# Kernel tuning notes

Hardware: AMD Instinct MI355X
Metric: run time of the kernel (lower is better)

## Reference

```python
import jax, jax.numpy as jnp
import numpy as np

N_HEADS = 16
ALIBI_BIAS_MAX = 8


def _alibi_bias(n_heads, seq_len):
    # MPT build_alibi_bias: bias[h, j] = -(seq_len-1-j) * slope_h, arranged [1,H,1,S]
    pos = jnp.arange(1 - seq_len, 1, dtype=jnp.float32).reshape(1, 1, 1, seq_len)
    m = jnp.arange(1, n_heads + 1, dtype=jnp.float32) * (ALIBI_BIAS_MAX / n_heads)
    slopes = (1.0 / jnp.exp2(m)).reshape(1, n_heads, 1, 1)
    return pos * slopes  # [1,H,1,S]


def setup_inputs() -> dict:
    key = jax.random.key(0)
    k1, k2, k3 = jax.random.split(key, 3)
    B, S, D = 1, 2048, 2048
    x = jax.random.normal(k1, (B, S, D), dtype=jnp.float32)
    # Wqkv: Linear(D, 3D, bias=False); out_proj: Linear(D, D, bias=False)
    w_qkv = jax.random.normal(k2, (3 * D, D), dtype=jnp.float32) * (1.0 / np.sqrt(D))
    w_out = jax.random.normal(k3, (D, D), dtype=jnp.float32) * (1.0 / np.sqrt(D))
    return {"x": x, "w_qkv": w_qkv, "w_out": w_out}


def reference(x, w_qkv, w_out):
    B, S, D = x.shape
    H = N_HEADS
    d = D // H
    qkv = x @ w_qkv.T                              # [B,S,3D]
    q, k, v = jnp.split(qkv, 3, axis=-1)
    q = q.reshape(B, S, H, d).transpose(0, 2, 1, 3)  # [B,H,S,d]
    k = k.reshape(B, S, H, d).transpose(0, 2, 1, 3)
    v = v.reshape(B, S, H, d).transpose(0, 2, 1, 3)
    scale = 1.0 / np.sqrt(d)
    scores = jnp.einsum('bhqd,bhkd->bhqk', q, k) * scale  # [B,H,S,S]
    scores = scores + _alibi_bias(H, S)
    min_val = jnp.finfo(scores.dtype).min
    causal = jnp.tril(jnp.ones((S, S), dtype=bool))
    scores = jnp.where(causal[None, None, :, :], scores, min_val)
    probs = jax.nn.softmax(scores.astype(jnp.float32), axis=-1).astype(q.dtype)
    out = jnp.einsum('bhqk,bhkd->bhqd', probs, v)  # [B,H,S,d]
    out = out.transpose(0, 2, 1, 3).reshape(B, S, D)
    return out @ w_out.T
```

## Files before the change

### kernel.cpp

```cpp
#include <hip/hip_runtime.h>

typedef __bf16 bf16;
typedef __bf16 bf16x8 __attribute__((ext_vector_type(8)));
typedef __bf16 bf16x4 __attribute__((ext_vector_type(4)));
typedef float f32x4 __attribute__((ext_vector_type(4)));

#if __has_builtin(__builtin_amdgcn_exp2f)
#define EXP2(x) __builtin_amdgcn_exp2f(x)
#else
#define EXP2(x) exp2f(x)
#endif

__device__ __forceinline__ void gload_lds16(const void* g, void* l) {
  __builtin_amdgcn_global_load_lds(
      (const __attribute__((address_space(1))) void*)g,
      (__attribute__((address_space(3))) void*)l, 16, 0, 0);
}

__global__ __launch_bounds__(256) void cast_all(const float* __restrict__ x,
                                                const float* __restrict__ wqkv,
                                                const float* __restrict__ wout,
                                                bf16* __restrict__ x_bf,
                                                bf16* __restrict__ wqkv_bf,
                                                bf16* __restrict__ wout_bf) {
  const int b = blockIdx.x;
  const float* src;
  bf16* dst;
  int i;
  if (b < 4096) {
    src = x; dst = x_bf; i = b * 1024 + threadIdx.x * 4;
  } else if (b < 16384) {
    src = wqkv; dst = wqkv_bf; i = (b - 4096) * 1024 + threadIdx.x * 4;
  } else {
    src = wout; dst = wout_bf; i = (b - 16384) * 1024 + threadIdx.x * 4;
  }
  float4 v = *(const float4*)(src + i);
  bf16x4 o = {(bf16)v.x, (bf16)v.y, (bf16)v.z, (bf16)v.w};
  *(bf16x4*)(dst + i) = o;
}

__global__ __launch_bounds__(256) void gemm1_qkv(const bf16* __restrict__ A,
                                                 const bf16* __restrict__ B,
                                                 bf16* __restrict__ qb,
                                                 bf16* __restrict__ kb,
                                                 bf16* __restrict__ vt) {
  constexpr int K = 2048;
  __shared__ bf16 As[128 * 32];
  __shared__ bf16 Bs[128 * 32];
  const int t = threadIdx.x;
  const int w = t >> 6, l = t & 63;
  const int lr = l & 15, lg = l >> 4;
  const int nwg = 768;
  int lin = blockIdx.y * 48 + blockIdx.x;
  lin = (lin & 7) * (nwg >> 3) + (lin >> 3);
  const int bn = lin % 48;
  const int bm = lin / 48;
  const int wr = w >> 1, wc = w & 1;

  f32x4 acc[4][4] = {};
  const int row0 = t >> 2;
  const int cc0 = (t & 3) * 8;

  for (int k0 = 0; k0 < K; k0 += 32) {
#pragma unroll
    for (int r = 0; r < 2; ++r) {
      const int row = r * 64 + row0;
      gload_lds16(A + (size_t)(bm * 128 + row) * K + k0 + cc0,
                  (char*)As + (r * 256 + w * 64) * 16);
      gload_lds16(B + (size_t)(bn * 128 + row) * K + k0 + cc0,
                  (char*)Bs + (r * 256 + w * 64) * 16);
    }
    __syncthreads();
    bf16x8 af[4], bfr[4];
#pragma unroll
    for (int i = 0; i < 4; ++i) {
      af[i] = *(const bf16x8*)((const char*)As + (wr * 64 + i * 16 + lr) * 64 + lg * 16);
      bfr[i] = *(const bf16x8*)((const char*)Bs + (wc * 64 + i * 16 + lr) * 64 + lg * 16);
    }
#pragma unroll
    for (int mi = 0; mi < 4; ++mi)
#pragma unroll
      for (int ni = 0; ni < 4; ++ni)
        acc[mi][ni] = __builtin_amdgcn_mfma_f32_16x16x32_bf16(af[mi], bfr[ni],
                                                              acc[mi][ni], 0, 0, 0);
    __syncthreads();
  }

  const int mb = bm * 128 + wr * 64 + lg * 4;
  const int nb = bn * 128 + wc * 64 + lr;
  if (bn * 128 < 4096) {
    bf16* dst = (bn * 128 < 2048) ? qb : kb;
#pragma unroll
    for (int mi = 0; mi < 4; ++mi) {
      const int mg = mb + mi * 16;
#pragma unroll
      for (int ni = 0; ni < 4; ++ni) {
        const int ng = (nb + ni * 16) & 2047;
#pragma unroll
        for (int rr = 0; rr < 4; ++rr)
          dst[(size_t)(mg + rr) * 2048 + ng] = (bf16)acc[mi][ni][rr];
      }
    }
  } else {
#pragma unroll
    for (int mi = 0; mi < 4; ++mi) {
      const int mg = mb + mi * 16;
#pragma unroll
      for (int ni = 0; ni < 4; ++ni) {
        const int dc = nb + ni * 16 - 4096;
        bf16x4 pk = {(bf16)acc[mi][ni][0], (bf16)acc[mi][ni][1],
                     (bf16)acc[mi][ni][2], (bf16)acc[mi][ni][3]};
        *(bf16x4*)(vt + (size_t)dc * 2048 + mg) = pk;
      }
    }
  }
}

__global__ __launch_bounds__(256) void gemm2_64x128(const bf16* __restrict__ A,
                                                    const bf16* __restrict__ B,
                                                    float* __restrict__ Cf) {
  constexpr int K = 2048, N = 2048;
  __shared__ bf16 As[64 * 32];
  __shared__ bf16 Bs[128 * 32];
  const int t = threadIdx.x;
  const int w = t >> 6, l = t & 63;
  const int lr = l & 15, lg = l >> 4;
  int lin = blockIdx.y * 16 + blockIdx.x;
  lin = (lin & 7) * 64 + (lin >> 3);
  const int bn = lin % 16;
  const int bm = lin / 16;

  f32x4 acc[4][2] = {};

  for (int k0 = 0; k0 < K; k0 += 32) {
    {
      const int row = t >> 2;
      gload_lds16(A + (size_t)(bm * 64 + row) * K + k0 + (t & 3) * 8,
                  (char*)As + (w * 64) * 16);
    }
#pragma unroll
    for (int r = 0; r < 2; ++r) {
      const int c = r * 256 + t;
      const int row = c >> 2;
      gload_lds16(B + (size_t)(bn * 128 + row) * K + k0 + (c & 3) * 8,
                  (char*)Bs + (r * 256 + w * 64) * 16);
    }
    __syncthreads();
    bf16x8 af[4], bfr[2];
#pragma unroll
    for (int i = 0; i < 4; ++i)
      af[i] = *(const bf16x8*)((const char*)As + (i * 16 + lr) * 64 + lg * 16);
#pragma unroll
    for (int i = 0; i < 2; ++i)
      bfr[i] = *(const bf16x8*)((const char*)Bs + (w * 32 + i * 16 + lr) * 64 + lg * 16);
#pragma unroll
    for (int mi = 0; mi < 4; ++mi)
#pragma unroll
      for (int ni = 0; ni < 2; ++ni)
        acc[mi][ni] = __builtin_amdgcn_mfma_f32_16x16x32_bf16(af[mi], bfr[ni],
                                                              acc[mi][ni], 0, 0, 0);
    __syncthreads();
  }

  const int mb = bm * 64 + lg * 4;
  const int nb = bn * 128 + w * 32 + lr;
#pragma unroll
  for (int mi = 0; mi < 4; ++mi) {
    const int mg = mb + mi * 16;
#pragma unroll
    for (int ni = 0; ni < 2; ++ni) {
      const int ng = nb + ni * 16;
#pragma unroll
      for (int rr = 0; rr < 4; ++rr)
        Cf[(size_t)(mg + rr) * N + ng] = acc[mi][ni][rr];
    }
  }
}

__global__ __launch_bounds__(256) void attn_kernel(const bf16* __restrict__ qb,
                                                   const bf16* __restrict__ kb,
                                                   const bf16* __restrict__ vt,
                                                   bf16* __restrict__ out,
                                                   bf16* __restrict__ pA,
                                                   bf16* __restrict__ pB,
                                                   float* __restrict__ ml) {
  constexpr int S = 2048, D = 2048;
  __shared__ bf16 Ks[64 * 128];
  __shared__ bf16 Vs[128 * 64];
  __shared__ bf16 Ps[4][16 * 64];
  const int t = threadIdx.x;
  const int w = t >> 6, l = t & 63;
  const int lr = l & 15, lg = l >> 4;
  const int b = blockIdx.x;

  int h, qt, piece, ns;
  if (b < 1024) {
    const int j = b >> 2;
    h = j & 15; qt = 16 + (j >> 4); piece = b & 3; ns = 4;
  } else if (b < 1280) {
    const int j = (b - 1024) >> 1;
    h = j & 15; qt = 8 + (j >> 4); piece = (b - 1024) & 1; ns = 2;
  } else {
    const int i = b - 1280;
    h = i & 15; qt = i >> 4; piece = 0; ns = 1;
  }
  const bool split = (ns > 1);
  const int q0 = qt * 64;
  const float slope2 = exp2f(-0.5f * (float)(h + 1)) * 1.4426950408889634f;
  const float scale2 = 0.08838834764831845f * 1.4426950408889634f;
  const int W = (int)(24.0f / slope2);
  const int s0 = (q0 > W) ? ((q0 - W) >> 6) : 0;
  const int len = qt + 1 - s0;
  const int start = s0 + (len * piece) / ns;
  const int end = s0 + (len * (piece + 1)) / ns;

  bf16x8 qf[4];
  {
    const bf16* qrow = qb + (size_t)(q0 + w * 16 + lr) * D + h * 128 + lg * 8;
#pragma unroll
    for (int kk = 0; kk < 4; ++kk) qf[kk] = *(const bf16x8*)(qrow + kk * 32);
  }

  f32x4 ob[8] = {};
  float mrow[4] = {-1e30f, -1e30f, -1e30f, -1e30f};
  float lrow[4] = {0.f, 0.f, 0.f, 0.f};

  auto stage = [&](int kv0) {
#pragma unroll
    for (int r = 0; r < 4; ++r) {
      {
        const int krow = r * 16 + (t >> 4);
        const int kcc = t & 15;
        gload_lds16(kb + (size_t)(kv0 + krow) * D + h * 128 + ((kcc ^ (krow & 7)) * 8),
                    (char*)Ks + (r * 256 + w * 64) * 16);
      }
      {
        const int vrow = r * 32 + (t >> 3);
        const int vcc = t & 7;
        gload_lds16(vt + (size_t)(h * 128 + vrow) * S + kv0 + ((vcc ^ (vrow & 7)) * 8),
                    (char*)Vs + (r * 256 + w * 64) * 16);
      }
    }
  };

  for (int tile = start; tile < end; ++tile) {
    const int kv0 = tile << 6;
    stage(kv0);
    __syncthreads();

    f32x4 sc[4] = {};
    __builtin_amdgcn_s_setprio(1);
#pragma unroll
    for (int jb = 0; jb < 4; ++jb) {
      const int row = jb * 16 + lr;
#pragma unroll
      for (int kk = 0; kk < 4; ++kk) {
        const int byte = row * 256 + ((kk * 64 + lg * 16) ^ ((row & 7) << 4));
        bf16x8 kf = *(const bf16x8*)((const char*)Ks + byte);
        sc[jb] = __builtin_amdgcn_mfma_f32_16x16x32_bf16(qf[kk], kf, sc[jb], 0, 0, 0);
      }
    }
    __builtin_amdgcn_s_setprio(0);

    float bias[4];
#pragma unroll
    for (int jb = 0; jb < 4; ++jb)
      bias[jb] = slope2 * (float)(kv0 + jb * 16 + lr - (S - 1));
    const bool diag = (tile == qt);
    float xv[4][4], m2r[4];
#pragma unroll
    for (int rr = 0; rr < 4; ++rr) {
#pragma unroll
      for (int jb = 0; jb < 4; ++jb) {
        float v = fmaf(sc[jb][rr], scale2, bias[jb]);
        if (diag && (jb * 16 + lr > w * 16 + lg * 4 + rr)) v = -1e30f;
        xv[rr][jb] = v;
      }
      float m2 = fmaxf(fmaxf(xv[rr][0], xv[rr][1]), fmaxf(xv[rr][2], xv[rr][3]));
      m2 = fmaxf(m2, __shfl_xor(m2, 1));
      m2 = fmaxf(m2, __shfl_xor(m2, 2));
      m2 = fmaxf(m2, __shfl_xor(m2, 4));
      m2 = fmaxf(m2, __shfl_xor(m2, 8));
      m2r[rr] = m2;
    }
    float need = fmaxf(fmaxf(m2r[0] - mrow[0], m2r[1] - mrow[1]),
                       fmaxf(m2r[2] - mrow[2], m2r[3] - mrow[3]));
    if (!__all(need <= 8.0f)) {
#pragma unroll
      for (int rr = 0; rr < 4; ++rr) {
        const float mnew = fmaxf(mrow[rr], m2r[rr]);
        const float cf = EXP2(mrow[rr] - mnew);
        lrow[rr] *= cf;
        mrow[rr] = mnew;
#pragma unroll
        for (int db = 0; db < 8; ++db) ob[db][rr] *= cf;
      }
    }
    char* pbase = (char*)Ps[w];
#pragma unroll
    for (int rr = 0; rr < 4; ++rr) {
      const int prow = lg * 4 + rr;
      const int sw = (prow & 7) << 4;
      float ps = 0.f;
#pragma unroll
      for (int jb = 0; jb < 4; ++jb) {
        const float p = EXP2(xv[rr][jb] - mrow[rr]);
        *(bf16*)(pbase + ((prow * 128 + jb * 32 + lr * 2) ^ sw)) = (bf16)p;
        ps += p;
      }
      lrow[rr] += ps;
    }

    bf16x8 pf[2];
#pragma unroll
    for (int s = 0; s < 2; ++s)
      pf[s] = *(const bf16x8*)(pbase + ((lr * 128 + s * 64 + lg * 16) ^ ((lr & 7) << 4)));
    __builtin_amdgcn_s_setprio(1);
#pragma unroll
    for (int db = 0; db < 8; ++db) {
      const int vrow = db * 16 + lr;
#pragma unroll
      for (int s = 0; s < 2; ++s) {
        const int byte = vrow * 128 + ((s * 64 + lg * 16) ^ ((vrow & 7) << 4));
        bf16x8 vf = *(const bf16x8*)((const char*)Vs + byte);
        ob[db] = __builtin_amdgcn_mfma_f32_16x16x32_bf16(pf[s], vf, ob[db], 0, 0, 0);
      }
    }
    __builtin_amdgcn_s_setprio(0);
    __syncthreads();
  }

  if (!split) {
#pragma unroll
    for (int rr = 0; rr < 4; ++rr) {
      float ls = lrow[rr];
      ls += __shfl_xor(ls, 1);
      ls += __shfl_xor(ls, 2);
      ls += __shfl_xor(ls, 4);
      ls += __shfl_xor(ls, 8);
      const float inv = 1.0f / ls;
      const int mg = q0 + w * 16 + lg * 4 + rr;
#pragma unroll
      for (int db = 0; db < 8; ++db)
        out[(size_t)mg * D + h * 128 + db * 16 + lr] = (bf16)(ob[db][rr] * inv);
    }
  } else {
    bf16* po = (b < 1024) ? pA + (size_t)b * 8192 : pB + (size_t)(b - 1024) * 8192;
#pragma unroll
    for (int rr = 0; rr < 4; ++rr) {
      float ls = lrow[rr];
      ls += __shfl_xor(ls, 1);
      ls += __shfl_xor(ls, 2);
      ls += __shfl_xor(ls, 4);
      ls += __shfl_xor(ls, 8);
      const int row = w * 16 + lg * 4 + rr;
#pragma unroll
      for (int db = 0; db < 8; ++db)
        po[row * 128 + db * 16 + lr] = (bf16)ob[db][rr];
      if (lr == 0) {
        ml[b * 128 + row] = mrow[rr];
        ml[b * 128 + 64 + row] = ls;
      }
    }
  }
}

__global__ __launch_bounds__(256) void attn_merge(const bf16* __restrict__ pA,
                                                  const bf16* __restrict__ pB,
                                                  const float* __restrict__ ml,
                                                  bf16* __restrict__ out) {
  const int j = blockIdx.x;
  const int t = threadIdx.x;
  int ns, c0, h, qt;
  if (j < 256) {
    ns = 4; c0 = 4 * j; h = j & 15; qt = 16 + (j >> 4);
  } else {
    const int j2 = j - 256;
    ns = 2; c0 = 1024 + 2 * j2; h = j2 & 15; qt = 8 + (j2 >> 4);
  }
  const int q0 = qt * 64;
  const int row = t >> 2;
  const int col0 = (t & 3) * 32;

  float m[4], lv[4];
  float M = -1e30f;
  for (int i = 0; i < ns; ++i) {
    m[i] = ml[(c0 + i) * 128 + row];
    lv[i] = ml[(c0 + i) * 128 + 64 + row];
    M = fmaxf(M, m[i]);
  }
  float wsum = 0.f, wgt[4];
  for (int i = 0; i < ns; ++i) {
    wgt[i] = EXP2(m[i] - M);
    wsum += wgt[i] * lv[i];
  }
  const float inv = 1.0f / wsum;

  float accv[32] = {};
  for (int i = 0; i < ns; ++i) {
    const int c = c0 + i;
    const bf16* po = (c < 1024) ? pA + (size_t)c * 8192 : pB + (size_t)(c - 1024) * 8192;
    const bf16* pr = po + row * 128 + col0;
    const float wi = wgt[i];
#pragma unroll
    for (int k = 0; k < 32; ++k) accv[k] += wi * (float)pr[k];
  }
  bf16* o = out + (size_t)(q0 + row) * 2048 + h * 128 + col0;
#pragma unroll
  for (int k = 0; k < 4; ++k) {
    bf16x8 o8;
#pragma unroll
    for (int e = 0; e < 8; ++e) o8[e] = (bf16)(accv[k * 8 + e] * inv);
    *(bf16x8*)(o + k * 8) = o8;
  }
}

extern "C" void kernel_launch(void* const* d_in, const int* in_sizes, int n_in,
                              void* d_out, int out_size, void* d_ws, size_t ws_size,
                              hipStream_t stream) {
  (void)in_sizes; (void)n_in; (void)out_size; (void)ws_size;
  const float* x = (const float*)d_in[0];
  const float* wqkv = (const float*)d_in[1];
  const float* wout = (const float*)d_in[2];
  float* out = (float*)d_out;

  bf16* x_bf = (bf16*)d_ws;
  bf16* wqkv_bf = x_bf + (size_t)2048 * 2048;
  bf16* wout_bf = wqkv_bf + (size_t)6144 * 2048;
  bf16* qb = wout_bf + (size_t)2048 * 2048;
  bf16* kb = qb + (size_t)2048 * 2048;
  bf16* vt = kb + (size_t)2048 * 2048;
  bf16* attn = wqkv_bf;
  bf16* pA = wqkv_bf + (size_t)2048 * 2048;
  bf16* pB = x_bf;
  float* ml = (float*)((char*)d_ws + (size_t)4 * 1024 * 1024);

  cast_all<<<20480, 256, 0, stream>>>(x, wqkv, wout, x_bf, wqkv_bf, wout_bf);
  gemm1_qkv<<<dim3(48, 16), 256, 0, stream>>>(x_bf, wqkv_bf, qb, kb, vt);
  attn_kernel<<<1408, 256, 0, stream>>>(qb, kb, vt, attn, pA, pB, ml);
  attn_merge<<<384, 256, 0, stream>>>(pA, pB, ml, attn);
  gemm2_64x128<<<dim3(16, 32), 256, 0, stream>>>(attn, wout_bf, out);
}
```

Measured before the change: 168.4 us.

## Double attention query tile to 128 rows with 8 waves per block

Each attention block now covers 128 query rows with 512 threads (8 waves) instead of 64 rows with 4 waves, so every staged K/V tile in LDS is reused by twice as many queries. The block-to-work mapping, split counts, per-element causal masking, partial buffer strides and merge kernel are all rewritten for the larger tile. This halves K/V global traffic per query, but gives coarser blocks and fewer of them, which can hurt load balance, and the causal mask is now evaluated on every tile rather than only the diagonal one.

```diff
diff --git a/kernel.cpp b/kernel.cpp
--- a/kernel.cpp
+++ b/kernel.cpp
@@ -177,7 +177,7 @@
   }
 }
 
-__global__ __launch_bounds__(256) void attn_kernel(const bf16* __restrict__ qb,
+__global__ __launch_bounds__(512) void attn_kernel(const bf16* __restrict__ qb,
                                                    const bf16* __restrict__ kb,
                                                    const bf16* __restrict__ vt,
                                                    bf16* __restrict__ out,
@@ -187,32 +187,34 @@
   constexpr int S = 2048, D = 2048;
   __shared__ bf16 Ks[64 * 128];
   __shared__ bf16 Vs[128 * 64];
-  __shared__ bf16 Ps[4][16 * 64];
+  __shared__ bf16 Ps[8][16 * 64];
   const int t = threadIdx.x;
   const int w = t >> 6, l = t & 63;
   const int lr = l & 15, lg = l >> 4;
   const int b = blockIdx.x;
 
-  int h, qt, piece, ns;
-  if (b < 1024) {
+  int h, qt2, piece, ns;
+  if (b < 512) {
     const int j = b >> 2;
-    h = j & 15; qt = 16 + (j >> 4); piece = b & 3; ns = 4;
-  } else if (b < 1280) {
-    const int j = (b - 1024) >> 1;
-    h = j & 15; qt = 8 + (j >> 4); piece = (b - 1024) & 1; ns = 2;
+    h = j & 15; qt2 = 8 + (j >> 4); piece = b & 3; ns = 4;
+  } else if (b < 704) {
+    const int u = b - 512;
+    const int j = u >> 1;
+    h = j & 15; qt2 = 2 + (j >> 4); piece = u & 1; ns = 2;
   } else {
-    const int i = b - 1280;
-    h = i & 15; qt = i >> 4; piece = 0; ns = 1;
+    const int i = b - 704;
+    h = i & 15; qt2 = i >> 4; piece = 0; ns = 1;
   }
   const bool split = (ns > 1);
-  const int q0 = qt * 64;
+  const int q0 = qt2 * 128;
   const float slope2 = exp2f(-0.5f * (float)(h + 1)) * 1.4426950408889634f;
   const float scale2 = 0.08838834764831845f * 1.4426950408889634f;
   const int W = (int)(24.0f / slope2);
   const int s0 = (q0 > W) ? ((q0 - W) >> 6) : 0;
-  const int len = qt + 1 - s0;
+  const int endt = 2 * qt2 + 2;
+  const int len = endt - s0;
   const int start = s0 + (len * piece) / ns;
-  const int end = s0 + (len * (piece + 1)) / ns;
+  const int pend = s0 + (len * (piece + 1)) / ns;
 
   bf16x8 qf[4];
   {
@@ -227,23 +229,24 @@
 
   auto stage = [&](int kv0) {
 #pragma unroll
-    for (int r = 0; r < 4; ++r) {
-      {
-        const int krow = r * 16 + (t >> 4);
-        const int kcc = t & 15;
-        gload_lds16(kb + (size_t)(kv0 + krow) * D + h * 128 + ((kcc ^ (krow & 7)) * 8),
-                    (char*)Ks + (r * 256 + w * 64) * 16);
-      }
-      {
-        const int vrow = r * 32 + (t >> 3);
-        const int vcc = t & 7;
-        gload_lds16(vt + (size_t)(h * 128 + vrow) * S + kv0 + ((vcc ^ (vrow & 7)) * 8),
-                    (char*)Vs + (r * 256 + w * 64) * 16);
-      }
+    for (int r = 0; r < 2; ++r) {
+      const int c = r * 512 + t;
+      const int krow = c >> 4;
+      const int kcc = c & 15;
+      gload_lds16(kb + (size_t)(kv0 + krow) * D + h * 128 + ((kcc ^ (krow & 7)) * 8),
+                  (char*)Ks + (r * 512 + w * 64) * 16);
+    }
+#pragma unroll
+    for (int r = 0; r < 2; ++r) {
+      const int c = r * 512 + t;
+      const int vrow = c >> 3;
+      const int vcc = c & 7;
+      gload_lds16(vt + (size_t)(h * 128 + vrow) * S + kv0 + ((vcc ^ (vrow & 7)) * 8),
+                  (char*)Vs + (r * 512 + w * 64) * 16);
     }
   };
 
-  for (int tile = start; tile < end; ++tile) {
+  for (int tile = start; tile < pend; ++tile) {
     const int kv0 = tile << 6;
     stage(kv0);
     __syncthreads();
@@ -266,14 +269,14 @@
 #pragma unroll
     for (int jb = 0; jb < 4; ++jb)
       bias[jb] = slope2 * (float)(kv0 + jb * 16 + lr - (S - 1));
-    const bool diag = (tile == qt);
     float xv[4][4], m2r[4];
 #pragma unroll
     for (int rr = 0; rr < 4; ++rr) {
+      const int i = q0 + w * 16 + lg * 4 + rr;
 #pragma unroll
       for (int jb = 0; jb < 4; ++jb) {
         float v = fmaf(sc[jb][rr], scale2, bias[jb]);
-        if (diag && (jb * 16 + lr > w * 16 + lg * 4 + rr)) v = -1e30f;
+        if (kv0 + jb * 16 + lr > i) v = -1e30f;
         xv[rr][jb] = v;
       }
       float m2 = fmaxf(fmaxf(xv[rr][0], xv[rr][1]), fmaxf(xv[rr][2], xv[rr][3]));
@@ -345,7 +348,7 @@
         out[(size_t)mg * D + h * 128 + db * 16 + lr] = (bf16)(ob[db][rr] * inv);
     }
   } else {
-    bf16* po = (b < 1024) ? pA + (size_t)b * 8192 : pB + (size_t)(b - 1024) * 8192;
+    bf16* po = (b < 512) ? pA + (size_t)b * 16384 : pB + (size_t)(b - 512) * 16384;
 #pragma unroll
     for (int rr = 0; rr < 4; ++rr) {
       float ls = lrow[rr];
@@ -358,8 +361,8 @@
       for (int db = 0; db < 8; ++db)
         po[row * 128 + db * 16 + lr] = (bf16)ob[db][rr];
       if (lr == 0) {
-        ml[b * 128 + row] = mrow[rr];
-        ml[b * 128 + 64 + row] = ls;
+        ml[b * 256 + row] = mrow[rr];
+        ml[b * 256 + 128 + row] = ls;
       }
     }
   }
@@ -371,47 +374,51 @@
                                                   bf16* __restrict__ out) {
   const int j = blockIdx.x;
   const int t = threadIdx.x;
-  int ns, c0, h, qt;
-  if (j < 256) {
-    ns = 4; c0 = 4 * j; h = j & 15; qt = 16 + (j >> 4);
+  int ns, c0, h, qt2;
+  if (j < 128) {
+    ns = 4; c0 = 4 * j; h = j & 15; qt2 = 8 + (j >> 4);
   } else {
-    const int j2 = j - 256;
-    ns = 2; c0 = 1024 + 2 * j2; h = j2 & 15; qt = 8 + (j2 >> 4);
-  }
-  const int q0 = qt * 64;
-  const int row = t >> 2;
+    const int j2 = j - 128;
+    ns = 2; c0 = 512 + 2 * j2; h = j2 & 15; qt2 = 2 + (j2 >> 4);
+  }
+  const int q0 = qt2 * 128;
+  const int row0 = t >> 2;
   const int col0 = (t & 3) * 32;
 
-  float m[4], lv[4];
-  float M = -1e30f;
-  for (int i = 0; i < ns; ++i) {
-    m[i] = ml[(c0 + i) * 128 + row];
-    lv[i] = ml[(c0 + i) * 128 + 64 + row];
-    M = fmaxf(M, m[i]);
-  }
-  float wsum = 0.f, wgt[4];
-  for (int i = 0; i < ns; ++i) {
-    wgt[i] = EXP2(m[i] - M);
-    wsum += wgt[i] * lv[i];
-  }
-  const float inv = 1.0f / wsum;
-
-  float accv[32] = {};
-  for (int i = 0; i < ns; ++i) {
-    const int c = c0 + i;
-    const bf16* po = (c < 1024) ? pA + (size_t)c * 8192 : pB + (size_t)(c - 1024) * 8192;
-    const bf16* pr = po + row * 128 + col0;
-    const float wi = wgt[i];
-#pragma unroll
-    for (int k = 0; k < 32; ++k) accv[k] += wi * (float)pr[k];
-  }
-  bf16* o = out + (size_t)(q0 + row) * 2048 + h * 128 + col0;
-#pragma unroll
-  for (int k = 0; k < 4; ++k) {
-    bf16x8 o8;
-#pragma unroll
-    for (int e = 0; e < 8; ++e) o8[e] = (bf16)(accv[k * 8 + e] * inv);
-    *(bf16x8*)(o + k * 8) = o8;
+  for (int rg = 0; rg < 2; ++rg) {
+    const int row = row0 + rg * 64;
+    float m[4], lv[4];
+    float M = -1e30f;
+    for (int i = 0; i < ns; ++i) {
+      m[i] = ml[(c0 + i) * 256 + row];
+      lv[i] = ml[(c0 + i) * 256 + 128 + row];
+      M = fmaxf(M, m[i]);
+    }
+    float wsum = 0.f, wgt[4];
+    for (int i = 0; i < ns; ++i) {
+      wgt[i] = EXP2(m[i] - M);
+      wsum += wgt[i] * lv[i];
+    }
+    const float inv = 1.0f / wsum;
+
+    float accv[32] = {};
+    for (int i = 0; i < ns; ++i) {
+      const int c = c0 + i;
+      const bf16* po =
+          (c < 512) ? pA + (size_t)c * 16384 : pB + (size_t)(c - 512) * 16384;
+      const bf16* pr = po + row * 128 + col0;
+      const float wi = wgt[i];
+#pragma unroll
+      for (int k = 0; k < 32; ++k) accv[k] += wi * (float)pr[k];
+    }
+    bf16* o = out + (size_t)(q0 + row) * 2048 + h * 128 + col0;
+#pragma unroll
+    for (int k = 0; k < 4; ++k) {
+      bf16x8 o8;
+#pragma unroll
+      for (int e = 0; e < 8; ++e) o8[e] = (bf16)(accv[k * 8 + e] * inv);
+      *(bf16x8*)(o + k * 8) = o8;
+    }
   }
 }
 
@@ -433,11 +440,11 @@
   bf16* attn = wqkv_bf;
   bf16* pA = wqkv_bf + (size_t)2048 * 2048;
   bf16* pB = x_bf;
-  float* ml = (float*)((char*)d_ws + (size_t)4 * 1024 * 1024);
+  float* ml = (float*)((char*)d_ws + (size_t)6 * 1024 * 1024);
 
   cast_all<<<20480, 256, 0, stream>>>(x, wqkv, wout, x_bf, wqkv_bf, wout_bf);
   gemm1_qkv<<<dim3(48, 16), 256, 0, stream>>>(x_bf, wqkv_bf, qb, kb, vt);
-  attn_kernel<<<1408, 256, 0, stream>>>(qb, kb, vt, attn, pA, pB, ml);
-  attn_merge<<<384, 256, 0, stream>>>(pA, pB, ml, attn);
+  attn_kernel<<<736, 512, 0, stream>>>(qb, kb, vt, attn, pA, pB, ml);
+  attn_merge<<<224, 256, 0, stream>>>(pA, pB, ml, attn);
   gemm2_64x128<<<dim3(16, 32), 256, 0, stream>>>(attn, wout_bf, out);
 }
```

Result: slower. 176.2 us (+4.6%).
